# Kernel optimization log

Hardware: AMD Instinct MI355X
Metric: run time of the kernel (lower is better)

Reference implementation:

```python
import jax, jax.numpy as jnp
import numpy as np

VOCAB = 65
N_EMBD = 32
HEAD = 16
BLOCK = 8
B = 65536


def setup_inputs() -> dict:
    key = jax.random.key(0)
    ks = jax.random.split(key, 12)
    idx = jax.random.randint(ks[0], (B, BLOCK), 0, VOCAB)
    targets = jax.random.randint(ks[1], (B, BLOCK), 0, VOCAB)
    s = 0.02
    tok_emb = jax.random.normal(ks[2], (VOCAB, N_EMBD), jnp.float32) * s
    pos_emb = jax.random.normal(ks[3], (BLOCK, N_EMBD), jnp.float32) * s
    Wk = jax.random.normal(ks[4], (N_EMBD, HEAD), jnp.float32) * s
    bk = jnp.zeros((HEAD,), jnp.float32)
    Wq = jax.random.normal(ks[5], (N_EMBD, HEAD), jnp.float32) * s
    bq = jnp.zeros((HEAD,), jnp.float32)
    Wv = jax.random.normal(ks[6], (N_EMBD, HEAD), jnp.float32) * s
    bv = jnp.zeros((HEAD,), jnp.float32)
    Wlm = jax.random.normal(ks[7], (HEAD, VOCAB), jnp.float32) * s
    blm = jnp.zeros((VOCAB,), jnp.float32)
    return {"idx": idx, "targets": targets, "tok_emb": tok_emb, "pos_emb": pos_emb,
            "Wk": Wk, "bk": bk, "Wq": Wq, "bq": bq, "Wv": Wv, "bv": bv,
            "Wlm": Wlm, "blm": blm}


def reference(idx, targets, tok_emb, pos_emb, Wk, bk, Wq, bq, Wv, bv, Wlm, blm):
    Bsz, T = idx.shape
    x = tok_emb[idx] + pos_emb[None, :T, :]                  # (B,T,C)
    k = x @ Wk + bk                                          # (B,T,H)
    q = x @ Wq + bq
    wei = jnp.einsum('bth,bsh->bts', q, k) * (HEAD ** -0.5)  # (B,T,T)
    tril = jnp.tril(jnp.ones((T, T), bool))
    wei = jnp.where(tril[None], wei, -jnp.inf)
    # NOTE: original torch code uses F.softmax(wei, dim=1) — over the QUERY axis.
    wei = jax.nn.softmax(wei, axis=1)
    v = x @ Wv + bv
    attn = jnp.einsum('bts,bsh->bth', wei, v)                # (B,T,H)
    logits = attn @ Wlm + blm                                # (B,T,V)
    logits_flat = logits.reshape(Bsz * T, VOCAB)
    tgt_flat = targets.reshape(Bsz * T)
    logp = jax.nn.log_softmax(logits_flat, axis=-1)
    loss = -jnp.mean(jnp.take_along_axis(logp, tgt_flat[:, None], axis=-1))
    return logits_flat, loss
```

## Files before the change

### kernel.cpp

```cpp
#include <hip/hip_runtime.h>

#define NVOC 65
#define NE   32
#define HD   16
#define NB   65536
#define NROWS (NB * 8)
#define NLOG  (NROWS * NVOC)


static __device__ __forceinline__ float readlane_f(float v, int l) {
  return __uint_as_float(__builtin_amdgcn_readlane(__float_as_uint(v), l));
}

__global__ __launch_bounds__(1024) void bigram_tables(
    const float* __restrict__ tok, const float* __restrict__ pos,
    const float* __restrict__ Wk, const float* __restrict__ bk,
    const float* __restrict__ Wq, const float* __restrict__ bq,
    const float* __restrict__ Wv, const float* __restrict__ bv,
    const float* __restrict__ Wlm, float* __restrict__ ws)
{
  __shared__ float S[8416];
  const int tid = threadIdx.x;
  const int bid = blockIdx.x;
  if (bid == 0 && tid == 0) {
    ws[0] = 0.f;
    ((unsigned int*)ws)[1] = 0u;
  }
  for (int o = tid; o < 2080; o += 1024) S[o] = tok[o];
  for (int o = tid; o < 256;  o += 1024) S[2080 + o] = pos[o];
  for (int o = tid; o < 512;  o += 1024) {
    S[2336 + o] = Wq[o]; S[2848 + o] = Wk[o]; S[3360 + o] = Wv[o];
  }
  for (int o = tid; o < 1040; o += 1024) S[3872 + o] = Wlm[o];
  __syncthreads();

  for (int o = tid; o < 1168; o += 1024) {
    if (o < 1040) {
      const int a = o >> 4, h = o & 15;
      float sq = 0.f, sk = 0.f, sv = 0.f;
      #pragma unroll
      for (int c = 0; c < NE; ++c) {
        const float e = S[a*32 + c];
        sq = fmaf(e, S[2336 + c*16 + h], sq);
        sk = fmaf(e, S[2848 + c*16 + h], sk);
        sv = fmaf(e, S[3360 + c*16 + h], sv);
      }
      S[4912 + o] = sq; S[5952 + o] = sk; S[6992 + o] = sv;
    } else {
      const int o2 = o - 1040, t = o2 >> 4, h = o2 & 15;
      float sq = bq[h], sk = bk[h], sv = bv[h];
      #pragma unroll
      for (int c = 0; c < NE; ++c) {
        const float e = S[2080 + t*32 + c];
        sq = fmaf(e, S[2336 + c*16 + h], sq);
        sk = fmaf(e, S[2848 + c*16 + h], sk);
        sv = fmaf(e, S[3360 + c*16 + h], sv);
      }
      S[8032 + o2] = sq; S[8160 + o2] = sk; S[8288 + o2] = sv;
    }
  }
  __syncthreads();

  float* wsTab = ws + 16;
  const int lo = bid * 632;
  const int hi = (lo + 632 < 10074) ? lo + 632 : 10074;
  for (int o = lo + tid; o < hi; o += 1024) {
    float r = 0.f; int dst;
    if (o < 4225) {
      const int a = o / 65, b = o % 65;
      #pragma unroll
      for (int h = 0; h < HD; ++h) r = fmaf(S[4912 + a*16 + h], S[5952 + b*16 + h], r);
      r *= 0.25f; dst = o;
    } else if (o < 4745) {
      const int o2 = o - 4225, a = o2 >> 3, s2 = o2 & 7;
      #pragma unroll
      for (int h = 0; h < HD; ++h) r = fmaf(S[4912 + a*16 + h], S[8160 + s2*16 + h], r);
      r *= 0.25f; dst = 8450 + o2;
    } else if (o < 5265) {
      const int o2 = o - 4745, t2 = o2 / 65, b = o2 % 65;
      #pragma unroll
      for (int h = 0; h < HD; ++h) r = fmaf(S[8032 + t2*16 + h], S[5952 + b*16 + h], r);
      r *= 0.25f; dst = 8970 + o2;
    } else if (o < 5329) {
      const int o2 = o - 5265, t2 = o2 >> 3, s2 = o2 & 7;
      #pragma unroll
      for (int h = 0; h < HD; ++h) r = fmaf(S[8032 + t2*16 + h], S[8160 + s2*16 + h], r);
      r *= 0.25f; dst = 9490 + o2;
    } else if (o < 9554) {
      const int o2 = o - 5329, a = o2 / 65, j = o2 % 65;
      #pragma unroll
      for (int h = 0; h < HD; ++h) r = fmaf(S[6992 + a*16 + h], S[3872 + h*65 + j], r);
      dst = 4225 + o2;
    } else {
      const int o2 = o - 9554, s2 = o2 / 65, j = o2 % 65;
      #pragma unroll
      for (int h = 0; h < HD; ++h) r = fmaf(S[8288 + s2*16 + h], S[3872 + h*65 + j], r);
      dst = o;
    }
    wsTab[dst] = r;
  }
}

__global__ __launch_bounds__(512, 8) void bigram_main(
    const int* __restrict__ idx, const int* __restrict__ tgt,
    const float* __restrict__ blm, float* __restrict__ ws,
    float* __restrict__ out)
{
  __shared__ __align__(16) float S[10074];
  __shared__ float red[8];
  const int tid = threadIdx.x;
  const int lane = tid & 63;
  const int w    = tid >> 6;
  const int t    = lane >> 3;
  const int s    = lane & 7;
  const int u    = lane & 7;
  const int gw = blockIdx.x * 8 + w;
  const int iv = idx[gw*64 + lane];
  const int tv = tgt[gw*64 + lane];
  const float blmj  = blm[lane];
  const float blm64 = blm[64];
  const float* wsTab = ws + 16;
  {
    const float4* t4 = (const float4*)wsTab;
    float4* s4 = (float4*)S;
    for (int o = tid; o < 2518; o += 512) s4[o] = t4[o];
    if (tid < 2) S[10072 + tid] = wsTab[10072 + tid];
  }
  __syncthreads();

  const float g4 = S[9490 + lane];
  float pvl[8], pvl64[8];
  #pragma unroll
  for (int k = 0; k < 8; ++k) {
    pvl[k]   = S[9554 + k*65 + lane];
    pvl64[k] = S[9554 + k*65 + 64];
  }
  const bool b0 = (lane & 1) != 0, b1 = (lane & 2) != 0, b2 = (lane & 4) != 0;

  float acc_lsm = 0.f, acc_tl = 0.f;
  for (int itb = 0; itb < 8; ++itb) {
    const int base = itb * 8;
    const int av  = __shfl(iv, base + s);
    const int a_t = __shfl(iv, base + t);
    float wr = S[a_t*65 + av] + S[8450 + a_t*8 + s] + S[8970 + t*65 + av] + g4;
    float e = (t >= s) ? __expf(wr) : 0.f;
    float sm = e;
    sm += __shfl_xor(sm, 8); sm += __shfl_xor(sm, 16); sm += __shfl_xor(sm, 32);
    const float wsm = __fdividef(e, sm);
    float Ms[8], Ms64[8];
    #pragma unroll
    for (int k = 0; k < 8; ++k) {
      const int ak = __builtin_amdgcn_readlane(iv, base + k);
      Ms[k]   = S[4225 + ak*65 + lane] + pvl[k];
      Ms64[k] = S[4225 + ak*65 + 64]  + pvl64[k];
    }
    float lg64v = blm64;
    #pragma unroll
    for (int k = 0; k < 8; ++k) {
      const float wk_row = __shfl(wsm, u*8 + k);
      lg64v = fmaf(wk_row, Ms64[k], lg64v);
    }
    const int rowbase = (gw*8 + itb) * 520;
    if (lane < 8) out[rowbase + lane*65 + 64] = lg64v;
    float ee[8];
    #pragma unroll
    for (int tt = 0; tt < 8; ++tt) {
      float lg = blmj;
      #pragma unroll
      for (int k = 0; k <= tt; ++k) {
        const float wk = readlane_f(wsm, tt*8 + k);
        lg = fmaf(wk, Ms[k], lg);
      }
      out[rowbase + tt*65 + lane] = lg;
      ee[tt] = __expf(lg);
      const int tg  = __builtin_amdgcn_readlane(tv, base + tt);
      const int tgc = tg < 64 ? tg : 0;
      const float l_at_tg = readlane_f(lg, tgc);
      const float l64t    = readlane_f(lg64v, tt);
      acc_tl += (tg < 64) ? l_at_tg : l64t;
    }
    float k0 = b0 ? ee[1] : ee[0], s0 = b0 ? ee[0] : ee[1];
    float k1 = b0 ? ee[3] : ee[2], s1 = b0 ? ee[2] : ee[3];
    float k2 = b0 ? ee[5] : ee[4], s2 = b0 ? ee[4] : ee[5];
    float k3 = b0 ? ee[7] : ee[6], s3 = b0 ? ee[6] : ee[7];
    k0 += __shfl_xor(s0, 1); k1 += __shfl_xor(s1, 1);
    k2 += __shfl_xor(s2, 1); k3 += __shfl_xor(s3, 1);
    float m0 = b1 ? k1 : k0, t0 = b1 ? k0 : k1;
    float m1 = b1 ? k3 : k2, t1 = b1 ? k2 : k3;
    m0 += __shfl_xor(t0, 2); m1 += __shfl_xor(t1, 2);
    float r = b2 ? m1 : m0,  t2 = b2 ? m0 : m1;
    r += __shfl_xor(t2, 4);
    if (lane < 8) r += __expf(lg64v);
    r += __shfl_xor(r, 8); r += __shfl_xor(r, 16); r += __shfl_xor(r, 32);
    acc_lsm += __log2f(r);
  }
  float v = acc_lsm * (0.6931471805599453f * 0.125f) - acc_tl * 0.015625f;
  v += __shfl_xor(v, 1); v += __shfl_xor(v, 2);  v += __shfl_xor(v, 4);
  v += __shfl_xor(v, 8); v += __shfl_xor(v, 16); v += __shfl_xor(v, 32);
  if (lane == 0) red[w] = v;
  __syncthreads();
  if (tid == 0) {
    const float p = red[0] + red[1] + red[2] + red[3]
                  + red[4] + red[5] + red[6] + red[7];
    atomicAdd(&ws[0], p);
    __threadfence();
    const unsigned int old = atomicAdd(&((unsigned int*)ws)[1], 1u);
    if (old == 1023u) {
      const float tot = atomicAdd(&ws[0], 0.0f);
      out[NLOG] = tot * (1.0f / (float)NROWS);
    }
  }
}

extern "C" void kernel_launch(void* const* d_in, const int* in_sizes, int n_in,
                              void* d_out, int out_size, void* d_ws, size_t ws_size,
                              hipStream_t stream) {
  const int* idx = (const int*)d_in[0];
  const int* tgt = (const int*)d_in[1];
  float* ws = (float*)d_ws;
  float* out = (float*)d_out;

  bigram_tables<<<16, 1024, 0, stream>>>((const float*)d_in[2], (const float*)d_in[3],
                                         (const float*)d_in[4], (const float*)d_in[5],
                                         (const float*)d_in[6], (const float*)d_in[7],
                                         (const float*)d_in[8], (const float*)d_in[9],
                                         (const float*)d_in[10], ws);
  bigram_main<<<1024, 512, 0, stream>>>(idx, tgt, (const float*)d_in[11], ws, out);
}
```

Measured before the change: 225.3 us.

## Software-pipeline next batch's attention softmax and replace atomic loss reduction with finalize kernel

Moves the next batch's attention-weight gather, exp, and cross-lane sum into the current iteration, interleaving the shuffle reductions between halves of the logit loop to hide latency. Also removes the global atomic accumulation and last-block counter: each block writes a partial loss to workspace, and a third single-block kernel sums them deterministically. This drops atomic contention and fence cost but adds one kernel launch and slightly more register pressure in the main loop.

```diff
diff --git a/kernel.cpp b/kernel.cpp
--- a/kernel.cpp
+++ b/kernel.cpp
@@ -22,10 +22,6 @@
   __shared__ float S[8416];
   const int tid = threadIdx.x;
   const int bid = blockIdx.x;
-  if (bid == 0 && tid == 0) {
-    ws[0] = 0.f;
-    ((unsigned int*)ws)[1] = 0u;
-  }
   for (int o = tid; o < 2080; o += 1024) S[o] = tok[o];
   for (int o = tid; o < 256;  o += 1024) S[2080 + o] = pos[o];
   for (int o = tid; o < 512;  o += 1024) {
@@ -103,8 +99,8 @@
 
 __global__ __launch_bounds__(512, 8) void bigram_main(
     const int* __restrict__ idx, const int* __restrict__ tgt,
-    const float* __restrict__ blm, float* __restrict__ ws,
-    float* __restrict__ out)
+    const float* __restrict__ blm, const float* __restrict__ ws,
+    float* __restrict__ wsout, float* __restrict__ out)
 {
   __shared__ __align__(16) float S[10074];
   __shared__ float red[8];
@@ -137,38 +133,53 @@
   }
   const bool b0 = (lane & 1) != 0, b1 = (lane & 2) != 0, b2 = (lane & 4) != 0;
 
-  float acc_lsm = 0.f, acc_tl = 0.f;
-  for (int itb = 0; itb < 8; ++itb) {
-    const int base = itb * 8;
-    const int av  = __shfl(iv, base + s);
-    const int a_t = __shfl(iv, base + t);
+  float wsm_cur;
+  {
+    const int av  = __shfl(iv, s);
+    const int a_t = __shfl(iv, t);
     float wr = S[a_t*65 + av] + S[8450 + a_t*8 + s] + S[8970 + t*65 + av] + g4;
     float e = (t >= s) ? __expf(wr) : 0.f;
     float sm = e;
     sm += __shfl_xor(sm, 8); sm += __shfl_xor(sm, 16); sm += __shfl_xor(sm, 32);
-    const float wsm = __fdividef(e, sm);
-    float Ms[8], Ms64[8];
+    wsm_cur = __fdividef(e, sm);
+  }
+
+  float acc_lsm = 0.f, acc_tl = 0.f;
+  for (int itb = 0; itb < 8; ++itb) {
+    const int base  = itb * 8;
+    const int basen = ((itb + 1) & 7) * 8;
+    float msr[8], Ms64[8];
     #pragma unroll
     for (int k = 0; k < 8; ++k) {
       const int ak = __builtin_amdgcn_readlane(iv, base + k);
-      Ms[k]   = S[4225 + ak*65 + lane] + pvl[k];
-      Ms64[k] = S[4225 + ak*65 + 64]  + pvl64[k];
-    }
+      msr[k]  = S[4225 + ak*65 + lane];
+      Ms64[k] = S[4225 + ak*65 + 64] + pvl64[k];
+    }
+    const int av_n  = __shfl(iv, basen + s);
+    const int a_tn  = __shfl(iv, basen + t);
+    float Ms[8];
+    #pragma unroll
+    for (int k = 0; k < 8; ++k) Ms[k] = msr[k] + pvl[k];
+    const float wr_n = S[a_tn*65 + av_n] + S[8450 + a_tn*8 + s]
+                     + S[8970 + t*65 + av_n] + g4;
+    float e_n = (t >= s) ? __expf(wr_n) : 0.f;
     float lg64v = blm64;
     #pragma unroll
     for (int k = 0; k < 8; ++k) {
-      const float wk_row = __shfl(wsm, u*8 + k);
+      const float wk_row = __shfl(wsm_cur, u*8 + k);
       lg64v = fmaf(wk_row, Ms64[k], lg64v);
     }
+    float sm_n = e_n;
+    sm_n += __shfl_xor(sm_n, 8);
     const int rowbase = (gw*8 + itb) * 520;
     if (lane < 8) out[rowbase + lane*65 + 64] = lg64v;
     float ee[8];
     #pragma unroll
-    for (int tt = 0; tt < 8; ++tt) {
+    for (int tt = 0; tt < 4; ++tt) {
       float lg = blmj;
       #pragma unroll
       for (int k = 0; k <= tt; ++k) {
-        const float wk = readlane_f(wsm, tt*8 + k);
+        const float wk = readlane_f(wsm_cur, tt*8 + k);
         lg = fmaf(wk, Ms[k], lg);
       }
       out[rowbase + tt*65 + lane] = lg;
@@ -179,6 +190,24 @@
       const float l64t    = readlane_f(lg64v, tt);
       acc_tl += (tg < 64) ? l_at_tg : l64t;
     }
+    sm_n += __shfl_xor(sm_n, 16);
+    #pragma unroll
+    for (int tt = 4; tt < 8; ++tt) {
+      float lg = blmj;
+      #pragma unroll
+      for (int k = 0; k <= tt; ++k) {
+        const float wk = readlane_f(wsm_cur, tt*8 + k);
+        lg = fmaf(wk, Ms[k], lg);
+      }
+      out[rowbase + tt*65 + lane] = lg;
+      ee[tt] = __expf(lg);
+      const int tg  = __builtin_amdgcn_readlane(tv, base + tt);
+      const int tgc = tg < 64 ? tg : 0;
+      const float l_at_tg = readlane_f(lg, tgc);
+      const float l64t    = readlane_f(lg64v, tt);
+      acc_tl += (tg < 64) ? l_at_tg : l64t;
+    }
+    sm_n += __shfl_xor(sm_n, 32);
     float k0 = b0 ? ee[1] : ee[0], s0 = b0 ? ee[0] : ee[1];
     float k1 = b0 ? ee[3] : ee[2], s1 = b0 ? ee[2] : ee[3];
     float k2 = b0 ? ee[5] : ee[4], s2 = b0 ? ee[4] : ee[5];
@@ -193,6 +222,7 @@
     if (lane < 8) r += __expf(lg64v);
     r += __shfl_xor(r, 8); r += __shfl_xor(r, 16); r += __shfl_xor(r, 32);
     acc_lsm += __log2f(r);
+    wsm_cur = __fdividef(e_n, sm_n);
   }
   float v = acc_lsm * (0.6931471805599453f * 0.125f) - acc_tl * 0.015625f;
   v += __shfl_xor(v, 1); v += __shfl_xor(v, 2);  v += __shfl_xor(v, 4);
@@ -200,15 +230,26 @@
   if (lane == 0) red[w] = v;
   __syncthreads();
   if (tid == 0) {
-    const float p = red[0] + red[1] + red[2] + red[3]
-                  + red[4] + red[5] + red[6] + red[7];
-    atomicAdd(&ws[0], p);
-    __threadfence();
-    const unsigned int old = atomicAdd(&((unsigned int*)ws)[1], 1u);
-    if (old == 1023u) {
-      const float tot = atomicAdd(&ws[0], 0.0f);
-      out[NLOG] = tot * (1.0f / (float)NROWS);
-    }
+    wsout[10112 + blockIdx.x] = red[0] + red[1] + red[2] + red[3]
+                              + red[4] + red[5] + red[6] + red[7];
+  }
+}
+
+__global__ __launch_bounds__(1024) void bigram_fin2(
+    const float* __restrict__ ws, float* __restrict__ out)
+{
+  __shared__ float r[16];
+  const int tid = threadIdx.x;
+  float v = ws[10112 + tid];
+  v += __shfl_xor(v, 1); v += __shfl_xor(v, 2);  v += __shfl_xor(v, 4);
+  v += __shfl_xor(v, 8); v += __shfl_xor(v, 16); v += __shfl_xor(v, 32);
+  if ((tid & 63) == 0) r[tid >> 6] = v;
+  __syncthreads();
+  if (tid == 0) {
+    float a = 0.f;
+    #pragma unroll
+    for (int i = 0; i < 16; ++i) a += r[i];
+    out[NLOG] = a * (1.0f / (float)NROWS);
   }
 }
 
@@ -225,5 +266,6 @@
                                          (const float*)d_in[6], (const float*)d_in[7],
                                          (const float*)d_in[8], (const float*)d_in[9],
                                          (const float*)d_in[10], ws);
-  bigram_main<<<1024, 512, 0, stream>>>(idx, tgt, (const float*)d_in[11], ws, out);
-}
+  bigram_main<<<1024, 512, 0, stream>>>(idx, tgt, (const float*)d_in[11], ws, ws, out);
+  bigram_fin2<<<1, 1024, 0, stream>>>(ws, out);
+}
```

After: 186.4 us. 17.3% less time.
